# Optimization experiments

Hardware: AMD Instinct MI355X
Metric: run time of the kernel (lower is better)

The kernel has to match this reference:

```python
import jax, jax.numpy as jnp
import numpy as np

D_MODEL = 1024
H = 16
D_K = 64
D_V = 64
D_G = D_MODEL // H  # 64, trignometric embedding
WAVE_LEN = 1000.0
B = 8
N = 512


def box_relational_embedding(boxes, dim_g=D_G):
    # boxes: (b, n, 4) as (x_min, y_min, x_max, y_max)
    x_min, y_min, x_max, y_max = jnp.split(boxes, 4, axis=-1)  # each (b, n, 1)
    cx = (x_min + x_max) * 0.5
    cy = (y_min + y_max) * 0.5
    w = (x_max - x_min) + 1.0
    h = (y_max - y_min) + 1.0
    # pairwise log-ratios, (b, n, n)
    delta_x = jnp.log(jnp.clip(jnp.abs((cx - jnp.swapaxes(cx, 1, 2)) / w), 1e-3, None))
    delta_y = jnp.log(jnp.clip(jnp.abs((cy - jnp.swapaxes(cy, 1, 2)) / h), 1e-3, None))
    delta_w = jnp.log(w / jnp.swapaxes(w, 1, 2))
    delta_h = jnp.log(h / jnp.swapaxes(h, 1, 2))
    pos = jnp.stack([delta_x, delta_y, delta_w, delta_h], axis=-1)  # (b, n, n, 4)
    n_freq = dim_g // 8
    feat_range = jnp.arange(n_freq, dtype=jnp.float32)
    dim_mat = 1.0 / (WAVE_LEN ** (feat_range / n_freq))  # (n_freq,)
    mul = (100.0 * pos)[..., None] * dim_mat  # (b, n, n, 4, n_freq)
    b, n = pos.shape[0], pos.shape[1]
    mul = mul.reshape(b, n, n, 4 * n_freq)
    return jnp.concatenate([jnp.sin(mul), jnp.cos(mul)], axis=-1)  # (b, n, n, dim_g)


def setup_inputs() -> dict:
    key = jax.random.key(0)
    ks = jax.random.split(key, 12)
    s = 0.02
    inp = {
        "queries": jax.random.normal(ks[0], (B, N, D_MODEL), jnp.float32),
        "keys": jax.random.normal(ks[1], (B, N, D_MODEL), jnp.float32),
        "values": jax.random.normal(ks[2], (B, N, D_MODEL), jnp.float32),
        "boxes": jax.random.uniform(ks[3], (B, N, 4), jnp.float32),
        "Wq": jax.random.normal(ks[4], (H * D_K, D_MODEL), jnp.float32) * s,
        "bq": jnp.zeros((H * D_K,), jnp.float32),
        "Wk": jax.random.normal(ks[5], (H * D_K, D_MODEL), jnp.float32) * s,
        "bk": jnp.zeros((H * D_K,), jnp.float32),
        "Wv": jax.random.normal(ks[6], (H * D_V, D_MODEL), jnp.float32) * s,
        "bv": jnp.zeros((H * D_V,), jnp.float32),
        "Wo": jax.random.normal(ks[7], (D_MODEL, H * D_V), jnp.float32) * s,
        "bo": jnp.zeros((D_MODEL,), jnp.float32),
        "Wg": jax.random.normal(ks[8], (H, D_G), jnp.float32) * s,  # h separate Linear(d_g,1) stacked
        "bg": jnp.zeros((H,), jnp.float32),
    }
    return inp


def reference(queries, keys, values, boxes, Wq, bq, Wk, bk, Wv, bv, Wo, bo, Wg, bg):
    b, nq, _ = queries.shape
    nk = keys.shape[1]
    # per-head geometry bias
    emb = box_relational_embedding(boxes)  # (b, nk, nk, D_G)
    g = jax.nn.relu(jnp.einsum('bnmd,hd->bhnm', emb, Wg) + bg[None, :, None, None])
    # QKV projections, split heads
    q = (queries @ Wq.T + bq).reshape(b, nq, H, D_K).transpose(0, 2, 1, 3)  # (b,h,nq,dk)
    k = (keys @ Wk.T + bk).reshape(b, nk, H, D_K).transpose(0, 2, 1, 3)    # (b,h,nk,dk)
    v = (values @ Wv.T + bv).reshape(b, nk, H, D_V).transpose(0, 2, 1, 3)  # (b,h,nk,dv)
    a = jnp.einsum('bhqd,bhkd->bhqk', q, k) / jnp.sqrt(jnp.float32(D_K))
    mn = jax.nn.softmax(jnp.log(jnp.clip(g, 1e-6, None)) + a, axis=-1)
    out = jnp.einsum('bhqk,bhkd->bqhd', mn, v).reshape(b, nq, H * D_V)
    return out @ Wo.T + bo
```

## Files before the change

### kernel.cpp

```cpp
#include <hip/hip_runtime.h>
#include <hip/hip_bf16.h>
#include <hip/hip_fp16.h>

typedef __attribute__((ext_vector_type(8))) short bf16x8;
typedef __attribute__((ext_vector_type(8))) _Float16 f16x8;
typedef __attribute__((ext_vector_type(4))) float f32x4;
typedef __attribute__((ext_vector_type(8))) short short8;

__device__ __forceinline__ short f2bf(float x) {
    unsigned u = __builtin_bit_cast(unsigned, x);
    u += 0x7fffu + ((u >> 16) & 1u);
    return (short)(u >> 16);
}

__device__ __forceinline__ void load_lds16(const void* g, void* l) {
    __builtin_amdgcn_global_load_lds((const __attribute__((address_space(1))) unsigned int*)g,
                                     (__attribute__((address_space(3))) unsigned int*)l, 16, 0, 0);
}

__global__ void convert_qkv(const float* __restrict__ q, const float* __restrict__ k,
                            const float* __restrict__ v, short* __restrict__ qo,
                            short* __restrict__ ko, short* __restrict__ vo) {
    int i = blockIdx.x * 256 + threadIdx.x;
    const float* s = blockIdx.y == 0 ? q : blockIdx.y == 1 ? k : v;
    short* d = blockIdx.y == 0 ? qo : blockIdx.y == 1 ? ko : vo;
    float4 val = reinterpret_cast<const float4*>(s)[i];
    short4 o; o.x = f2bf(val.x); o.y = f2bf(val.y); o.z = f2bf(val.z); o.w = f2bf(val.w);
    reinterpret_cast<short4*>(d)[i] = o;
}

__global__ void convert_w4(const float* __restrict__ w0, const float* __restrict__ w1,
                           const float* __restrict__ w2, const float* __restrict__ w3,
                           short* __restrict__ o0, short* __restrict__ o1,
                           short* __restrict__ o2, short* __restrict__ o3) {
    int i = blockIdx.x * 256 + threadIdx.x;
    const float* s = blockIdx.y == 0 ? w0 : blockIdx.y == 1 ? w1 : blockIdx.y == 2 ? w2 : w3;
    short* d = blockIdx.y == 0 ? o0 : blockIdx.y == 1 ? o1 : blockIdx.y == 2 ? o2 : o3;
    float4 val = reinterpret_cast<const float4*>(s)[i];
    short4 o; o.x = f2bf(val.x); o.y = f2bf(val.y); o.z = f2bf(val.z); o.w = f2bf(val.w);
    reinterpret_cast<short4*>(d)[i] = o;
}

__global__ void convert_f32_f16(const float* __restrict__ src, _Float16* __restrict__ dst, int n) {
    int i = blockIdx.x * blockDim.x + threadIdx.x;
    if (i < n) dst[i] = (_Float16)src[i];
}

__global__ void geom_kernel2(const float* __restrict__ boxes, const _Float16* __restrict__ Wgh,
                             const float* __restrict__ bg, __half* __restrict__ G) {
    const int tid = threadIdx.x;
    const int wave = tid >> 6, lane = tid & 63, quad = lane >> 4, l16 = lane & 15;
    const int m0 = blockIdx.x * 64;
    const int n = blockIdx.y;
    const int b = blockIdx.z;

    __shared__ __align__(16) _Float16 feat[4][16][72];
    __shared__ __align__(16) _Float16 gbuf[16][68];

    const int p = lane >> 2, c = lane & 3;
    const int m = m0 + wave * 16 + p;

    float4 bn = reinterpret_cast<const float4*>(boxes)[b * 512 + n];
    float4 bm = reinterpret_cast<const float4*>(boxes)[b * 512 + m];
    float cxn = (bn.x + bn.z) * 0.5f, cyn = (bn.y + bn.w) * 0.5f;
    float wn = bn.z - bn.x + 1.0f, hn = bn.w - bn.y + 1.0f;
    float cxm = (bm.x + bm.z) * 0.5f, cym = (bm.y + bm.w) * 0.5f;
    float wm = bm.z - bm.x + 1.0f, hm = bm.w - bm.y + 1.0f;

    float r;
    if (c == 0)      r = fmaxf(fabsf((cxn - cxm) / wn), 1e-3f);
    else if (c == 1) r = fmaxf(fabsf((cyn - cym) / hn), 1e-3f);
    else if (c == 2) r = wn / wm;
    else             r = hn / hm;
    float pos = __logf(r) * 100.0f;

    const float dm[8] = {1.0f, 0.42169651f, 0.17782794f, 0.07498942f,
                         0.03162278f, 0.01333521f, 0.00562341f, 0.00237137f};
    f16x8 sv8, cv8;
    #pragma unroll
    for (int f = 0; f < 8; ++f) {
        float th = pos * dm[f];
        sv8[f] = (_Float16)__sinf(th);
        cv8[f] = (_Float16)__cosf(th);
    }
    *(f16x8*)&feat[wave][p][c * 8]      = sv8;
    *(f16x8*)&feat[wave][p][32 + c * 8] = cv8;

    __syncthreads();

    f16x8 a0 = *(const f16x8*)&feat[wave][l16][quad * 8];
    f16x8 a1 = *(const f16x8*)&feat[wave][l16][32 + quad * 8];
    f16x8 b0 = *(const f16x8*)(Wgh + l16 * 64 + quad * 8);
    f16x8 b1 = *(const f16x8*)(Wgh + l16 * 64 + 32 + quad * 8);
    f32x4 acc = (f32x4){0.f, 0.f, 0.f, 0.f};
    acc = __builtin_amdgcn_mfma_f32_16x16x32_f16(a0, b0, acc, 0, 0, 0);
    acc = __builtin_amdgcn_mfma_f32_16x16x32_f16(a1, b1, acc, 0, 0, 0);

    float bgv = bg[l16];
    #pragma unroll
    for (int rr = 0; rr < 4; ++rr) {
        float g = fmaxf(acc[rr] + bgv, 1e-6f);
        gbuf[l16][wave * 16 + quad * 4 + rr] = (_Float16)g;
    }
    __syncthreads();

    const int h = tid >> 4, seg = tid & 15;
    ushort4 v = *(const ushort4*)&gbuf[h][seg * 4];
    *(ushort4*)&G[((long)((b * 16 + h) * 512 + n)) * 512 + m0 + seg * 4] = v;
}

__global__ __launch_bounds__(256, 3)
void proj_all3(const short* __restrict__ qkbf, const short* __restrict__ wqkb,
               const short* __restrict__ wvb, const short* __restrict__ vbf,
               const float* __restrict__ bq, const float* __restrict__ bk,
               const float* __restrict__ bv,
               short* __restrict__ QKh, _Float16* __restrict__ Vt) {
    __shared__ __align__(16) short As[4096];
    __shared__ __align__(16) short Bs[4096];
    const int tid = threadIdx.x;
    const int wave = tid >> 6, lane = tid & 63, quad = lane >> 4, l16 = lane & 15;
    const int bid = blockIdx.x;

    const short *Ap, *Bp;
    int m0, n0, z = 0;
    bool isV = bid >= 512;
    if (!isV) {
        z = bid >> 8;
        int t = bid & 255;
        n0 = (t & 7) * 128; m0 = (t >> 3) * 128;
        Ap = qkbf + (long)z * 4194304 + (long)m0 * 1024;
        Bp = wqkb + (long)z * 1048576 + (long)n0 * 1024;
    } else {
        int t = bid - 512;
        n0 = (t & 31) * 128; m0 = (t >> 5) * 128;
        Ap = wvb + (long)m0 * 1024;
        Bp = vbf + (long)n0 * 1024;
    }

    f32x4 acc[4][4];
    #pragma unroll
    for (int mg = 0; mg < 4; ++mg)
        #pragma unroll
        for (int ng = 0; ng < 4; ++ng) acc[mg][ng] = (f32x4){0.f, 0.f, 0.f, 0.f};

    const int r0 = tid >> 2, kk = (tid & 3) * 8;
    const short* ga0 = Ap + (long)r0 * 1024 + kk;
    const short* ga1 = Ap + (long)(64 + r0) * 1024 + kk;
    const short* gb0 = Bp + (long)r0 * 1024 + kk;
    const short* gb1 = Bp + (long)(64 + r0) * 1024 + kk;
    short* la0 = As + wave * 512;
    short* la1 = As + 2048 + wave * 512;
    short* lb0 = Bs + wave * 512;
    short* lb1 = Bs + 2048 + wave * 512;

    const int wr = wave >> 1, wc = wave & 1;

    for (int k0 = 0; k0 < 1024; k0 += 32) {
        load_lds16(ga0 + k0, la0);
        load_lds16(ga1 + k0, la1);
        load_lds16(gb0 + k0, lb0);
        load_lds16(gb1 + k0, lb1);
        __syncthreads();
        bf16x8 a[4], bb[4];
        #pragma unroll
        for (int g = 0; g < 4; ++g)
            a[g] = *(const bf16x8*)&As[(wr * 64 + g * 16 + l16) * 32 + quad * 8];
        #pragma unroll
        for (int g = 0; g < 4; ++g)
            bb[g] = *(const bf16x8*)&Bs[(wc * 64 + g * 16 + l16) * 32 + quad * 8];
        #pragma unroll
        for (int mg = 0; mg < 4; ++mg)
            #pragma unroll
            for (int ng = 0; ng < 4; ++ng)
                acc[mg][ng] = __builtin_amdgcn_mfma_f32_16x16x32_bf16(a[mg], bb[ng], acc[mg][ng], 0, 0, 0);
        __syncthreads();
    }

    #pragma unroll
    for (int mg = 0; mg < 4; ++mg)
        #pragma unroll
        for (int ng = 0; ng < 4; ++ng)
            #pragma unroll
            for (int r = 0; r < 4; ++r) {
                int row = m0 + wr * 64 + mg * 16 + quad * 4 + r;
                int col = n0 + wc * 64 + ng * 16 + l16;
                if (!isV) {
                    float v = acc[mg][ng][r] + (z ? bk[col] : bq[col]);
                    QKh[(long)z * 4194304 + (long)row * 1024 + col] = f2bf(v);
                } else {
                    float v = acc[mg][ng][r] + bv[row];
                    int bcol = col >> 9, lc = col & 511;
                    Vt[(long)bcol * 524288 + (long)row * 512 + lc] = (_Float16)v;
                }
            }
}

__global__ __launch_bounds__(256, 4)
void flash_attn6(const short* __restrict__ Q, const short* __restrict__ Kh,
                 const _Float16* __restrict__ Vt, const __half* __restrict__ G,
                 short* __restrict__ O) {
    const int tid = threadIdx.x;
    const int wave = tid >> 6, lane = tid & 63, quad = lane >> 4, l16 = lane & 15;
    const int qt = blockIdx.x, h = blockIdx.y, b = blockIdx.z;

    __shared__ __align__(16) short    Ks[64][72];
    __shared__ __align__(16) _Float16 Vs[64][72];
    __shared__ __align__(16) _Float16 Gs[64][72];
    __shared__ __align__(16) _Float16 Pbuf[4][16][72];

    const int qrow = qt * 64 + wave * 16;
    const long qoff = ((long)(b * 512 + qrow + l16)) * 1024 + h * 64 + quad * 8;
    bf16x8 aq0 = *(const bf16x8*)(Q + qoff);
    bf16x8 aq1 = *(const bf16x8*)(Q + qoff + 32);

    const int sr0 = tid >> 3,         sc0 = (tid & 7) * 8;
    const int sr1 = (tid + 256) >> 3, sc1 = ((tid + 256) & 7) * 8;
    const short* Kbase = Kh + (long)(b * 512) * 1024 + h * 64;
    const _Float16* Vbase = Vt + (long)b * 524288 + (long)(h * 64) * 512;
    const _Float16* Gbase = (const _Float16*)G + ((long)((b * 16 + h) * 512 + qt * 64)) * 512;

    f32x4 oacc[4];
    #pragma unroll
    for (int r = 0; r < 4; ++r) oacc[r] = (f32x4){0.f, 0.f, 0.f, 0.f};
    float rs = 0.f;

    for (int kt = 0; kt < 8; ++kt) {
        __syncthreads();
        short8 k0 = *(const short8*)(Kbase + (long)(kt * 64 + sr0) * 1024 + sc0);
        short8 k1 = *(const short8*)(Kbase + (long)(kt * 64 + sr1) * 1024 + sc1);
        short8 v0 = *(const short8*)(Vbase + (long)sr0 * 512 + kt * 64 + sc0);
        short8 v1 = *(const short8*)(Vbase + (long)sr1 * 512 + kt * 64 + sc1);
        short8 g0 = *(const short8*)(Gbase + (long)sr0 * 512 + kt * 64 + sc0);
        short8 g1 = *(const short8*)(Gbase + (long)sr1 * 512 + kt * 64 + sc1);
        *(short8*)&Ks[sr0][sc0] = k0;
        *(short8*)&Ks[sr1][sc1] = k1;
        *(short8*)&Vs[sr0][sc0] = v0;
        *(short8*)&Vs[sr1][sc1] = v1;
        *(short8*)&Gs[sr0][sc0] = g0;
        *(short8*)&Gs[sr1][sc1] = g1;
        __syncthreads();

        f32x4 sc[4];
        #pragma unroll
        for (int nk = 0; nk < 4; ++nk) {
            bf16x8 bk0 = *(const bf16x8*)&Ks[nk * 16 + l16][quad * 8];
            bf16x8 bk1 = *(const bf16x8*)&Ks[nk * 16 + l16][32 + quad * 8];
            f32x4 s = (f32x4){0.f, 0.f, 0.f, 0.f};
            s = __builtin_amdgcn_mfma_f32_16x16x32_bf16(aq0, bk0, s, 0, 0, 0);
            s = __builtin_amdgcn_mfma_f32_16x16x32_bf16(aq1, bk1, s, 0, 0, 0);
            sc[nk] = s;
        }
        #pragma unroll
        for (int nk = 0; nk < 4; ++nk)
            #pragma unroll
            for (int r = 0; r < 4; ++r)
                Pbuf[wave][quad * 4 + r][nk * 16 + l16] = (_Float16)__expf(sc[nk][r] * 0.125f);
        f16x8 ep0 = *(const f16x8*)&Pbuf[wave][l16][quad * 8];
        f16x8 ep1 = *(const f16x8*)&Pbuf[wave][l16][32 + quad * 8];
        f16x8 gA = *(const f16x8*)&Gs[wave * 16 + l16][quad * 8];
        f16x8 gB = *(const f16x8*)&Gs[wave * 16 + l16][32 + quad * 8];
        f16x8 gp0 = ep0 * gA;
        f16x8 gp1 = ep1 * gB;
        float part = 0.f;
        #pragma unroll
        for (int j = 0; j < 8; ++j) part += (float)gp0[j] + (float)gp1[j];
        rs += part;
        #pragma unroll
        for (int n4 = 0; n4 < 4; ++n4) {
            f16x8 bv0 = *(const f16x8*)&Vs[n4 * 16 + l16][quad * 8];
            f16x8 bv1 = *(const f16x8*)&Vs[n4 * 16 + l16][32 + quad * 8];
            oacc[n4] = __builtin_amdgcn_mfma_f32_16x16x32_f16(gp0, bv0, oacc[n4], 0, 0, 0);
            oacc[n4] = __builtin_amdgcn_mfma_f32_16x16x32_f16(gp1, bv1, oacc[n4], 0, 0, 0);
        }
    }

    rs += __shfl_xor(rs, 16);
    rs += __shfl_xor(rs, 32);
    float li[4];
    #pragma unroll
    for (int r = 0; r < 4; ++r) li[r] = __shfl(rs, quad * 4 + r);

    #pragma unroll
    for (int n4 = 0; n4 < 4; ++n4)
        #pragma unroll
        for (int r = 0; r < 4; ++r) {
            float o = oacc[n4][r] / li[r];
            O[((long)(b * 512 + qrow + quad * 4 + r)) * 1024 + h * 64 + n4 * 16 + l16] = f2bf(o);
        }
}

__global__ __launch_bounds__(256, 4)
void gemm_out2(const short* __restrict__ Hd, const short* __restrict__ wob,
               const float* __restrict__ bo, float* __restrict__ out) {
    __shared__ __align__(16) short As[4096];
    __shared__ __align__(16) short Bs[2048];
    const int tid = threadIdx.x;
    const int wave = tid >> 6, lane = tid & 63, quad = lane >> 4, l16 = lane & 15;
    const int m0 = blockIdx.y * 128, n0 = blockIdx.x * 64;
    const short* Ap = Hd + (long)m0 * 1024;
    const short* Bp = wob + (long)n0 * 1024;

    f32x4 acc[2][4];
    #pragma unroll
    for (int mg = 0; mg < 2; ++mg)
        #pragma unroll
        for (int ng = 0; ng < 4; ++ng) acc[mg][ng] = (f32x4){0.f, 0.f, 0.f, 0.f};

    const int r0 = tid >> 2, kk = (tid & 3) * 8;
    const short* ga0 = Ap + (long)r0 * 1024 + kk;
    const short* ga1 = Ap + (long)(64 + r0) * 1024 + kk;
    const short* gb0 = Bp + (long)r0 * 1024 + kk;
    short* la0 = As + wave * 512;
    short* la1 = As + 2048 + wave * 512;
    short* lb0 = Bs + wave * 512;

    const int mw = wave * 32;

    for (int k0 = 0; k0 < 1024; k0 += 32) {
        load_lds16(ga0 + k0, la0);
        load_lds16(ga1 + k0, la1);
        load_lds16(gb0 + k0, lb0);
        __syncthreads();
        bf16x8 a[2], bb[4];
        #pragma unroll
        for (int g = 0; g < 2; ++g)
            a[g] = *(const bf16x8*)&As[(mw + g * 16 + l16) * 32 + quad * 8];
        #pragma unroll
        for (int g = 0; g < 4; ++g)
            bb[g] = *(const bf16x8*)&Bs[(g * 16 + l16) * 32 + quad * 8];
        #pragma unroll
        for (int mg = 0; mg < 2; ++mg)
            #pragma unroll
            for (int ng = 0; ng < 4; ++ng)
                acc[mg][ng] = __builtin_amdgcn_mfma_f32_16x16x32_bf16(a[mg], bb[ng], acc[mg][ng], 0, 0, 0);
        __syncthreads();
    }

    #pragma unroll
    for (int mg = 0; mg < 2; ++mg)
        #pragma unroll
        for (int ng = 0; ng < 4; ++ng)
            #pragma unroll
            for (int r = 0; r < 4; ++r) {
                int row = m0 + mw + mg * 16 + quad * 4 + r;
                int col = n0 + ng * 16 + l16;
                out[(long)row * 1024 + col] = acc[mg][ng][r] + bo[col];
            }
}

extern "C" void kernel_launch(void* const* d_in, const int* in_sizes, int n_in,
                              void* d_out, int out_size, void* d_ws, size_t ws_size,
                              hipStream_t stream) {
    const float* queries = (const float*)d_in[0];
    const float* keys    = (const float*)d_in[1];
    const float* values  = (const float*)d_in[2];
    const float* boxes   = (const float*)d_in[3];
    const float* bq = (const float*)d_in[5];
    const float* bk = (const float*)d_in[7];
    const float* bv = (const float*)d_in[9];
    const float* bo = (const float*)d_in[11];
    const float* Wg = (const float*)d_in[12];
    const float* bg = (const float*)d_in[13];

    char* ws = (char*)d_ws;
    short* qbf = (short*)(ws + 0);
    short* kbf = (short*)(ws + 8388608);
    short* vbf = (short*)(ws + 16777216);
    short* wqb = (short*)(ws + 25165824);
    short* wkb = (short*)(ws + 27262976);
    short* wvb = (short*)(ws + 29360128);
    short* wob = (short*)(ws + 31457280);
    short* Qh  = (short*)(ws + 33554432);
    _Float16* Vt = (_Float16*)(ws + 50331648);
    short* Hd  = (short*)(ws + 58720256);
    __half* G  = (__half*)(ws + 67108864);
    _Float16* Wgh = (_Float16*)(ws + 33554432);

    convert_qkv<<<dim3(4096, 3), 256, 0, stream>>>(queries, keys, values, qbf, kbf, vbf);
    convert_w4<<<dim3(1024, 4), 256, 0, stream>>>((const float*)d_in[4], (const float*)d_in[6],
                                                  (const float*)d_in[8], (const float*)d_in[10],
                                                  wqb, wkb, wvb, wob);
    convert_f32_f16<<<4, 256, 0, stream>>>(Wg, Wgh, 1024);

    geom_kernel2<<<dim3(8, 512, 8), 256, 0, stream>>>(boxes, Wgh, bg, G);

    proj_all3<<<768, 256, 0, stream>>>(qbf, wqb, wvb, vbf, bq, bk, bv, Qh, Vt);

    flash_attn6<<<dim3(8, 16, 8), 256, 0, stream>>>(Qh, Qh + 4194304, Vt, G, Hd);

    gemm_out2<<<dim3(16, 32), 256, 0, stream>>>(Hd, wob, bo, (float*)d_out);
}
```

Before: 271.9 us.

## Triple-buffer LDS in projection and output GEMMs; replace divisions with log differences

The QKV projection and output GEMMs now use a three-stage LDS ring with asynchronous global-to-LDS loads issued two tiles ahead. Each step has one barrier and a partial vmcnt wait, replacing the old load/sync/compute/sync loop, so memory latency is meant to overlap with MFMA work. The geometry kernel computes log(num) - log(den) with a clamp in log space instead of dividing and then taking a log, which avoids the division. This triples LDS use per block, which may lower occupancy, and the hand-written waitcnt counts must match the number of outstanding loads exactly.

```diff
diff --git a/kernel.cpp b/kernel.cpp
--- a/kernel.cpp
+++ b/kernel.cpp
@@ -46,7 +46,7 @@
     if (i < n) dst[i] = (_Float16)src[i];
 }
 
-__global__ void geom_kernel2(const float* __restrict__ boxes, const _Float16* __restrict__ Wgh,
+__global__ void geom_kernel3(const float* __restrict__ boxes, const _Float16* __restrict__ Wgh,
                              const float* __restrict__ bg, __half* __restrict__ G) {
     const int tid = threadIdx.x;
     const int wave = tid >> 6, lane = tid & 63, quad = lane >> 4, l16 = lane & 15;
@@ -67,12 +67,11 @@
     float cxm = (bm.x + bm.z) * 0.5f, cym = (bm.y + bm.w) * 0.5f;
     float wm = bm.z - bm.x + 1.0f, hm = bm.w - bm.y + 1.0f;
 
-    float r;
-    if (c == 0)      r = fmaxf(fabsf((cxn - cxm) / wn), 1e-3f);
-    else if (c == 1) r = fmaxf(fabsf((cyn - cym) / hn), 1e-3f);
-    else if (c == 2) r = wn / wm;
-    else             r = hn / hm;
-    float pos = __logf(r) * 100.0f;
+    float num = (c == 0) ? fabsf(cxn - cxm) : (c == 1) ? fabsf(cyn - cym) : (c == 2) ? wn : hn;
+    float den = (c == 0) ? wn : (c == 1) ? hn : (c == 2) ? wm : hm;
+    float lr = __logf(num) - __logf(den);
+    if (c < 2) lr = fmaxf(lr, -6.9077552790f);
+    float pos = lr * 100.0f;
 
     const float dm[8] = {1.0f, 0.42169651f, 0.17782794f, 0.07498942f,
                          0.03162278f, 0.01333521f, 0.00562341f, 0.00237137f};
@@ -109,14 +108,42 @@
     *(ushort4*)&G[((long)((b * 16 + h) * 512 + n)) * 512 + m0 + seg * 4] = v;
 }
 
+#define PROJ_COMP(BC)                                                                  \
+    {                                                                                  \
+        bf16x8 a_[4], bb_[4];                                                          \
+        _Pragma("unroll")                                                              \
+        for (int g = 0; g < 4; ++g)                                                    \
+            a_[g] = *(const bf16x8*)&As[BC][(wr * 64 + g * 16 + l16) * 32 + quad * 8]; \
+        _Pragma("unroll")                                                              \
+        for (int g = 0; g < 4; ++g)                                                    \
+            bb_[g] = *(const bf16x8*)&Bs[BC][(wc * 64 + g * 16 + l16) * 32 + quad * 8];\
+        _Pragma("unroll")                                                              \
+        for (int mg = 0; mg < 4; ++mg)                                                 \
+            _Pragma("unroll")                                                          \
+            for (int ng = 0; ng < 4; ++ng)                                             \
+                acc[mg][ng] = __builtin_amdgcn_mfma_f32_16x16x32_bf16(a_[mg], bb_[ng], acc[mg][ng], 0, 0, 0); \
+    }
+
+#define PROJ_STEP(T, BC, BS)                                                           \
+    {                                                                                  \
+        asm volatile("s_waitcnt vmcnt(4)" ::: "memory");                               \
+        __builtin_amdgcn_s_barrier();                                                  \
+        const int k1_ = ((T) + 2) * 32;                                                \
+        load_lds16(ga0 + k1_, &As[BS][wb]);                                            \
+        load_lds16(ga1 + k1_, &As[BS][2048 + wb]);                                     \
+        load_lds16(gb0 + k1_, &Bs[BS][wb]);                                            \
+        load_lds16(gb1 + k1_, &Bs[BS][2048 + wb]);                                     \
+        PROJ_COMP(BC)                                                                  \
+    }
+
 __global__ __launch_bounds__(256, 3)
-void proj_all3(const short* __restrict__ qkbf, const short* __restrict__ wqkb,
+void proj_all4(const short* __restrict__ qkbf, const short* __restrict__ wqkb,
                const short* __restrict__ wvb, const short* __restrict__ vbf,
                const float* __restrict__ bq, const float* __restrict__ bk,
                const float* __restrict__ bv,
                short* __restrict__ QKh, _Float16* __restrict__ Vt) {
-    __shared__ __align__(16) short As[4096];
-    __shared__ __align__(16) short Bs[4096];
+    __shared__ __align__(16) short As[3][4096];
+    __shared__ __align__(16) short Bs[3][4096];
     const int tid = threadIdx.x;
     const int wave = tid >> 6, lane = tid & 63, quad = lane >> 4, l16 = lane & 15;
     const int bid = blockIdx.x;
@@ -148,33 +175,29 @@
     const short* ga1 = Ap + (long)(64 + r0) * 1024 + kk;
     const short* gb0 = Bp + (long)r0 * 1024 + kk;
     const short* gb1 = Bp + (long)(64 + r0) * 1024 + kk;
-    short* la0 = As + wave * 512;
-    short* la1 = As + 2048 + wave * 512;
-    short* lb0 = Bs + wave * 512;
-    short* lb1 = Bs + 2048 + wave * 512;
-
+    const int wb = wave * 512;
     const int wr = wave >> 1, wc = wave & 1;
 
-    for (int k0 = 0; k0 < 1024; k0 += 32) {
-        load_lds16(ga0 + k0, la0);
-        load_lds16(ga1 + k0, la1);
-        load_lds16(gb0 + k0, lb0);
-        load_lds16(gb1 + k0, lb1);
-        __syncthreads();
-        bf16x8 a[4], bb[4];
-        #pragma unroll
-        for (int g = 0; g < 4; ++g)
-            a[g] = *(const bf16x8*)&As[(wr * 64 + g * 16 + l16) * 32 + quad * 8];
-        #pragma unroll
-        for (int g = 0; g < 4; ++g)
-            bb[g] = *(const bf16x8*)&Bs[(wc * 64 + g * 16 + l16) * 32 + quad * 8];
-        #pragma unroll
-        for (int mg = 0; mg < 4; ++mg)
-            #pragma unroll
-            for (int ng = 0; ng < 4; ++ng)
-                acc[mg][ng] = __builtin_amdgcn_mfma_f32_16x16x32_bf16(a[mg], bb[ng], acc[mg][ng], 0, 0, 0);
-        __syncthreads();
-    }
+    load_lds16(ga0, &As[0][wb]);
+    load_lds16(ga1, &As[0][2048 + wb]);
+    load_lds16(gb0, &Bs[0][wb]);
+    load_lds16(gb1, &Bs[0][2048 + wb]);
+    load_lds16(ga0 + 32, &As[1][wb]);
+    load_lds16(ga1 + 32, &As[1][2048 + wb]);
+    load_lds16(gb0 + 32, &Bs[1][wb]);
+    load_lds16(gb1 + 32, &Bs[1][2048 + wb]);
+
+    for (int tb = 0; tb < 30; tb += 3) {
+        PROJ_STEP(tb,     0, 2)
+        PROJ_STEP(tb + 1, 1, 0)
+        PROJ_STEP(tb + 2, 2, 1)
+    }
+    asm volatile("s_waitcnt vmcnt(4)" ::: "memory");
+    __builtin_amdgcn_s_barrier();
+    PROJ_COMP(0)
+    asm volatile("s_waitcnt vmcnt(0)" ::: "memory");
+    __builtin_amdgcn_s_barrier();
+    PROJ_COMP(1)
 
     #pragma unroll
     for (int mg = 0; mg < 4; ++mg)
@@ -289,11 +312,38 @@
         }
 }
 
+#define GOUT_COMP(BC)                                                                  \
+    {                                                                                  \
+        bf16x8 a_[2], bb_[4];                                                          \
+        _Pragma("unroll")                                                              \
+        for (int g = 0; g < 2; ++g)                                                    \
+            a_[g] = *(const bf16x8*)&As[BC][(mw + g * 16 + l16) * 32 + quad * 8];      \
+        _Pragma("unroll")                                                              \
+        for (int g = 0; g < 4; ++g)                                                    \
+            bb_[g] = *(const bf16x8*)&Bs[BC][(g * 16 + l16) * 32 + quad * 8];          \
+        _Pragma("unroll")                                                              \
+        for (int mg = 0; mg < 2; ++mg)                                                 \
+            _Pragma("unroll")                                                          \
+            for (int ng = 0; ng < 4; ++ng)                                             \
+                acc[mg][ng] = __builtin_amdgcn_mfma_f32_16x16x32_bf16(a_[mg], bb_[ng], acc[mg][ng], 0, 0, 0); \
+    }
+
+#define GOUT_STEP(T, BC, BS)                                                           \
+    {                                                                                  \
+        asm volatile("s_waitcnt vmcnt(3)" ::: "memory");                               \
+        __builtin_amdgcn_s_barrier();                                                  \
+        const int k1_ = ((T) + 2) * 32;                                                \
+        load_lds16(ga0 + k1_, &As[BS][wb]);                                            \
+        load_lds16(ga1 + k1_, &As[BS][2048 + wb]);                                     \
+        load_lds16(gb0 + k1_, &Bs[BS][wb]);                                            \
+        GOUT_COMP(BC)                                                                  \
+    }
+
 __global__ __launch_bounds__(256, 4)
-void gemm_out2(const short* __restrict__ Hd, const short* __restrict__ wob,
+void gemm_out3(const short* __restrict__ Hd, const short* __restrict__ wob,
                const float* __restrict__ bo, float* __restrict__ out) {
-    __shared__ __align__(16) short As[4096];
-    __shared__ __align__(16) short Bs[2048];
+    __shared__ __align__(16) short As[3][4096];
+    __shared__ __align__(16) short Bs[3][2048];
     const int tid = threadIdx.x;
     const int wave = tid >> 6, lane = tid & 63, quad = lane >> 4, l16 = lane & 15;
     const int m0 = blockIdx.y * 128, n0 = blockIdx.x * 64;
@@ -310,31 +360,27 @@
     const short* ga0 = Ap + (long)r0 * 1024 + kk;
     const short* ga1 = Ap + (long)(64 + r0) * 1024 + kk;
     const short* gb0 = Bp + (long)r0 * 1024 + kk;
-    short* la0 = As + wave * 512;
-    short* la1 = As + 2048 + wave * 512;
-    short* lb0 = Bs + wave * 512;
-
+    const int wb = wave * 512;
     const int mw = wave * 32;
 
-    for (int k0 = 0; k0 < 1024; k0 += 32) {
-        load_lds16(ga0 + k0, la0);
-        load_lds16(ga1 + k0, la1);
-        load_lds16(gb0 + k0, lb0);
-        __syncthreads();
-        bf16x8 a[2], bb[4];
-        #pragma unroll
-        for (int g = 0; g < 2; ++g)
-            a[g] = *(const bf16x8*)&As[(mw + g * 16 + l16) * 32 + quad * 8];
-        #pragma unroll
-        for (int g = 0; g < 4; ++g)
-            bb[g] = *(const bf16x8*)&Bs[(g * 16 + l16) * 32 + quad * 8];
-        #pragma unroll
-        for (int mg = 0; mg < 2; ++mg)
-            #pragma unroll
-            for (int ng = 0; ng < 4; ++ng)
-                acc[mg][ng] = __builtin_amdgcn_mfma_f32_16x16x32_bf16(a[mg], bb[ng], acc[mg][ng], 0, 0, 0);
-        __syncthreads();
-    }
+    load_lds16(ga0, &As[0][wb]);
+    load_lds16(ga1, &As[0][2048 + wb]);
+    load_lds16(gb0, &Bs[0][wb]);
+    load_lds16(ga0 + 32, &As[1][wb]);
+    load_lds16(ga1 + 32, &As[1][2048 + wb]);
+    load_lds16(gb0 + 32, &Bs[1][wb]);
+
+    for (int tb = 0; tb < 30; tb += 3) {
+        GOUT_STEP(tb,     0, 2)
+        GOUT_STEP(tb + 1, 1, 0)
+        GOUT_STEP(tb + 2, 2, 1)
+    }
+    asm volatile("s_waitcnt vmcnt(3)" ::: "memory");
+    __builtin_amdgcn_s_barrier();
+    GOUT_COMP(0)
+    asm volatile("s_waitcnt vmcnt(0)" ::: "memory");
+    __builtin_amdgcn_s_barrier();
+    GOUT_COMP(1)
 
     #pragma unroll
     for (int mg = 0; mg < 2; ++mg)
@@ -382,11 +428,11 @@
                                                   wqb, wkb, wvb, wob);
     convert_f32_f16<<<4, 256, 0, stream>>>(Wg, Wgh, 1024);
 
-    geom_kernel2<<<dim3(8, 512, 8), 256, 0, stream>>>(boxes, Wgh, bg, G);
-
-    proj_all3<<<768, 256, 0, stream>>>(qbf, wqb, wvb, vbf, bq, bk, bv, Qh, Vt);
+    geom_kernel3<<<dim3(8, 512, 8), 256, 0, stream>>>(boxes, Wgh, bg, G);
+
+    proj_all4<<<768, 256, 0, stream>>>(qbf, wqb, wvb, vbf, bq, bk, bv, Qh, Vt);
 
     flash_attn6<<<dim3(8, 16, 8), 256, 0, stream>>>(Qh, Qh + 4194304, Vt, G, Hd);
 
-    gemm_out2<<<dim3(16, 32), 256, 0, stream>>>(Hd, wob, bo, (float*)d_out);
-}
+    gemm_out3<<<dim3(16, 32), 256, 0, stream>>>(Hd, wob, bo, (float*)d_out);
+}
```

Result: no change. 269.5 us (-0.9%).
